# Kernel tuning notes

Hardware: AMD Instinct MI355X
Metric: run time of the kernel (lower is better)

The kernel has to match this reference:

```python
import jax, jax.numpy as jnp
import numpy as np

N_IN, M, CIN, COUT, KVOL = 200000, 600000, 128, 64, 4
BN_EPS = 1e-5


def setup_inputs() -> dict:
    key = jax.random.key(0)
    k1, k2 = jax.random.split(key, 2)
    # Rulebook: transposed conv with kernel=stride=2 means every input voxel i
    # produces KVOL=4 distinct candidate output coords; each output voxel is fed
    # by exactly one (input, kernel-offset) pair. Pick M of the N_IN*KVOL children.
    rng = np.random.RandomState(0)
    perm = rng.permutation(N_IN * KVOL)[:M]
    in_idx = (perm // KVOL).astype(np.int32)   # parent input voxel per output voxel
    kidx = (perm % KVOL).astype(np.int32)      # kernel offset id per output voxel
    feats = jax.random.normal(k1, (N_IN, CIN), jnp.float32)
    weight = jax.random.normal(k2, (KVOL, CIN, COUT), jnp.float32) * (1.0 / np.sqrt(CIN * KVOL))
    gamma = jnp.ones((COUT,), jnp.float32)
    beta = jnp.zeros((COUT,), jnp.float32)
    return dict(feats=feats, weight=weight, gamma=gamma, beta=beta,
                in_idx=jnp.asarray(in_idx), kidx=jnp.asarray(kidx))


def reference(feats, weight, gamma, beta, in_idx, kidx):
    # Sparse transposed conv: gather parent features, apply per-offset GEMM, select.
    gathered = feats[in_idx]                                  # [M, Cin]
    out = jnp.zeros((in_idx.shape[0], weight.shape[2]), feats.dtype)
    for k in range(weight.shape[0]):                          # KVOL=4 structurally distinct weights
        out = out + jnp.where((kidx == k)[:, None], gathered @ weight[k], 0.0)
    # BatchNorm1d (training-mode batch stats over voxel dim) + ReLU
    mean = out.mean(axis=0)
    var = out.var(axis=0)                                     # biased, as torch BN uses
    y = (out - mean) * jax.lax.rsqrt(var + BN_EPS) * gamma + beta
    return jax.nn.relu(y)
```

## Files before the change

### kernel.cpp

```cpp
#include <hip/hip_runtime.h>

#define CIN  128
#define COUT 64
#define KVOL 4
#define TP   128
#define BN_EPS 1e-5f

typedef __bf16 bf16x8 __attribute__((ext_vector_type(8)));
typedef float  f32x4  __attribute__((ext_vector_type(4)));
typedef float  f32x8  __attribute__((ext_vector_type(8)));


__global__ void k_prepw(const float* __restrict__ weight, __bf16* __restrict__ wfrag) {
  int id = blockIdx.x * 256 + threadIdx.x;
  int j  = id & 7;
  int l  = (id >> 3) & 63;
  int ks = (id >> 9) & 3;
  int f  = (id >> 11) & 3;
  int k  = id >> 13;
  int kk = ks * 32 + (l >> 4) * 8 + j;
  int n  = 4 * (l & 15) + f;
  wfrag[id] = (__bf16)weight[(k * CIN + kk) * COUT + n];
}

__global__ void k_fill(int4* __restrict__ p, long n4) {
  long i = (long)blockIdx.x * blockDim.x + threadIdx.x;
  long stride = (long)gridDim.x * blockDim.x;
  int4 v = make_int4(-1, -1, -1, -1);
  for (; i < n4; i += stride) p[i] = v;
}

__global__ void k_tbl(const int* __restrict__ in_idx, const int* __restrict__ kidx,
                      int M, int N_IN, int* __restrict__ tbl_t) {
  for (int m = blockIdx.x * blockDim.x + threadIdx.x; m < M;
       m += gridDim.x * blockDim.x)
    tbl_t[(kidx[m] & 3) * N_IN + in_idx[m]] = m;
}

__device__ inline int4 ld_mk(const int* __restrict__ tbl_t, int k, int N_IN, int pi) {
  int4 mk;
  if (pi + 3 < N_IN) {
    mk = *(const int4*)&tbl_t[k * N_IN + pi];
  } else {
    mk.x = (pi + 0 < N_IN) ? tbl_t[k * N_IN + pi + 0] : -1;
    mk.y = (pi + 1 < N_IN) ? tbl_t[k * N_IN + pi + 1] : -1;
    mk.z = (pi + 2 < N_IN) ? tbl_t[k * N_IN + pi + 2] : -1;
    mk.w = (pi + 3 < N_IN) ? tbl_t[k * N_IN + pi + 3] : -1;
  }
  return mk;
}

__global__ __launch_bounds__(256, 4)
void k_pass1(const float* __restrict__ feats, const int* __restrict__ tbl_t,
             const __bf16* __restrict__ wfrag, float* __restrict__ pbuf, int N_IN) {
  __shared__ float red[512];
  int t  = threadIdx.x;
  int w  = t >> 6, l = t & 63;
  int lr = l & 15, lg = l >> 4;
  int base = blockIdx.x * TP + w * 32;

  bf16x8 a[2][4];
  #pragma unroll
  for (int mf = 0; mf < 2; ++mf) {
    int row = base + mf * 16 + lr;
    bool vr = row < N_IN;
    const float* ap = feats + (long)(vr ? row : 0) * CIN + lg * 8;
    #pragma unroll
    for (int ks = 0; ks < 4; ++ks) {
      f32x8 fv = {0.f,0.f,0.f,0.f,0.f,0.f,0.f,0.f};
      if (vr) fv = *(const f32x8*)(ap + ks * 32);
      a[mf][ks] = __builtin_convertvector(fv, bf16x8);
    }
  }

  float s[4] = {0.f,0.f,0.f,0.f}, q[4] = {0.f,0.f,0.f,0.f};
  int pi0 = base + lg * 4;
  int pi1 = base + 16 + lg * 4;

  #pragma unroll 1
  for (int k = 0; k < KVOL; ++k) {
    int4 mk0 = ld_mk(tbl_t, k, N_IN, pi0);
    int4 mk1 = ld_mk(tbl_t, k, N_IN, pi1);
    const bf16x8* wp = (const bf16x8*)wfrag + k * 1024 + l;
    f32x4 acc[2][4];
    #pragma unroll
    for (int mf = 0; mf < 2; ++mf)
      #pragma unroll
      for (int f = 0; f < 4; ++f) acc[mf][f] = (f32x4){0.f, 0.f, 0.f, 0.f};
    #pragma unroll
    for (int ks = 0; ks < 4; ++ks)
      #pragma unroll
      for (int f = 0; f < 4; ++f) {
        bf16x8 b = wp[(f * 4 + ks) * 64];
        acc[0][f] = __builtin_amdgcn_mfma_f32_16x16x32_bf16(a[0][ks], b, acc[0][f], 0, 0, 0);
        acc[1][f] = __builtin_amdgcn_mfma_f32_16x16x32_bf16(a[1][ks], b, acc[1][f], 0, 0, 0);
      }
    #pragma unroll
    for (int mf = 0; mf < 2; ++mf) {
      int4 mk = mf ? mk1 : mk0;
      #pragma unroll
      for (int reg = 0; reg < 4; ++reg) {
        int m = (reg == 0) ? mk.x : (reg == 1) ? mk.y : (reg == 2) ? mk.z : mk.w;
        if (m >= 0) {
          #pragma unroll
          for (int f = 0; f < 4; ++f) {
            float vv = acc[mf][f][reg];
            s[f] += vv; q[f] += vv * vv;
          }
        }
      }
    }
  }

  #pragma unroll
  for (int f = 0; f < 4; ++f) {
    s[f] += __shfl_xor(s[f], 16); s[f] += __shfl_xor(s[f], 32);
    q[f] += __shfl_xor(q[f], 16); q[f] += __shfl_xor(q[f], 32);
  }
  float* redS = red;
  float* redQ = red + 256;
  if (lg == 0) {
    #pragma unroll
    for (int f = 0; f < 4; ++f) {
      redS[w * 64 + 4 * lr + f] = s[f];
      redQ[w * 64 + 4 * lr + f] = q[f];
    }
  }
  __syncthreads();
  if (t < 128) {
    int col = t & 63;
    const float* src = (t < 64) ? redS : redQ;
    float v = 0.f;
    #pragma unroll
    for (int g = 0; g < 4; ++g) v += src[g * 64 + col];
    pbuf[(long)blockIdx.x * 128 + t] = v;
  }
}

__global__ void k_stats(const float* __restrict__ pbuf, int nb,
                        float* __restrict__ gsum, float* __restrict__ gsq) {
  __shared__ float red[256];
  int j = blockIdx.x;
  float v = 0.f;
  for (int r = threadIdx.x; r < nb; r += blockDim.x)
    v += pbuf[(long)r * 128 + j];
  red[threadIdx.x] = v;
  __syncthreads();
  #pragma unroll
  for (int sft = 128; sft > 0; sft >>= 1) {
    if (threadIdx.x < sft) red[threadIdx.x] += red[threadIdx.x + sft];
    __syncthreads();
  }
  if (threadIdx.x == 0) {
    if (j < 64) gsum[j] = red[0];
    else        gsq[j - 64] = red[0];
  }
}

__global__ __launch_bounds__(256, 4)
void k_pass2(const float* __restrict__ feats, const int* __restrict__ tbl_t,
             const __bf16* __restrict__ wfrag, float* __restrict__ out,
             const float* __restrict__ gsum, const float* __restrict__ gsq,
             const float* __restrict__ gamma, const float* __restrict__ beta,
             int N_IN, int M) {
  int t  = threadIdx.x;
  int w  = t >> 6, l = t & 63;
  int lr = l & 15, lg = l >> 4;
  int base = blockIdx.x * TP + w * 32;

  float inv = 1.0f / (float)M;
  f32x4 sm = *(const f32x4*)&gsum[4 * lr];
  f32x4 sq = *(const f32x4*)&gsq[4 * lr];
  f32x4 ga = *(const f32x4*)&gamma[4 * lr];
  f32x4 be = *(const f32x4*)&beta[4 * lr];
  float sc[4], sh[4];
  #pragma unroll
  for (int f = 0; f < 4; ++f) {
    float mu = sm[f] * inv;
    float r  = rsqrtf(sq[f] * inv - mu * mu + BN_EPS);
    sc[f] = r * ga[f];
    sh[f] = be[f] - mu * sc[f];
  }

  bf16x8 a[2][4];
  #pragma unroll
  for (int mf = 0; mf < 2; ++mf) {
    int row = base + mf * 16 + lr;
    bool vr = row < N_IN;
    const float* ap = feats + (long)(vr ? row : 0) * CIN + lg * 8;
    #pragma unroll
    for (int ks = 0; ks < 4; ++ks) {
      f32x8 fv = {0.f,0.f,0.f,0.f,0.f,0.f,0.f,0.f};
      if (vr) fv = *(const f32x8*)(ap + ks * 32);
      a[mf][ks] = __builtin_convertvector(fv, bf16x8);
    }
  }

  int pi0 = base + lg * 4;
  int pi1 = base + 16 + lg * 4;

  #pragma unroll 1
  for (int k = 0; k < KVOL; ++k) {
    int4 mk0 = ld_mk(tbl_t, k, N_IN, pi0);
    int4 mk1 = ld_mk(tbl_t, k, N_IN, pi1);
    const bf16x8* wp = (const bf16x8*)wfrag + k * 1024 + l;
    f32x4 acc[2][4];
    #pragma unroll
    for (int mf = 0; mf < 2; ++mf)
      #pragma unroll
      for (int f = 0; f < 4; ++f) acc[mf][f] = (f32x4){0.f, 0.f, 0.f, 0.f};
    #pragma unroll
    for (int ks = 0; ks < 4; ++ks)
      #pragma unroll
      for (int f = 0; f < 4; ++f) {
        bf16x8 b = wp[(f * 4 + ks) * 64];
        acc[0][f] = __builtin_amdgcn_mfma_f32_16x16x32_bf16(a[0][ks], b, acc[0][f], 0, 0, 0);
        acc[1][f] = __builtin_amdgcn_mfma_f32_16x16x32_bf16(a[1][ks], b, acc[1][f], 0, 0, 0);
      }
    #pragma unroll
    for (int mf = 0; mf < 2; ++mf) {
      int4 mk = mf ? mk1 : mk0;
      #pragma unroll
      for (int reg = 0; reg < 4; ++reg) {
        int m = (reg == 0) ? mk.x : (reg == 1) ? mk.y : (reg == 2) ? mk.z : mk.w;
        if (m >= 0) {
          f32x4 v4;
          #pragma unroll
          for (int f = 0; f < 4; ++f)
            v4[f] = fmaxf(fmaf(acc[mf][f][reg], sc[f], sh[f]), 0.f);
          __builtin_nontemporal_store(v4, (f32x4*)&out[(long)m * COUT + 4 * lr]);
        }
      }
    }
  }
}

extern "C" void kernel_launch(void* const* d_in, const int* in_sizes, int n_in,
                              void* d_out, int out_size, void* d_ws, size_t ws_size,
                              hipStream_t stream) {
  const float* feats  = (const float*)d_in[0];
  const float* weight = (const float*)d_in[1];
  const float* gamma  = (const float*)d_in[2];
  const float* beta   = (const float*)d_in[3];
  const int*   in_idx = (const int*)d_in[4];
  const int*   kidx   = (const int*)d_in[5];
  int M    = in_sizes[4];
  int N_IN = in_sizes[0] / CIN;
  float* out = (float*)d_out;

  int nb = (N_IN + TP - 1) / TP;

  float*  gsum  = (float*)((char*)d_ws + 128);
  float*  gsq   = (float*)((char*)d_ws + 384);
  __bf16* wfrag = (__bf16*)((char*)d_ws + 1024);
  int*    tbl_t = (int*)((char*)d_ws + 66560);
  size_t  pbuf_off = 66560 + (size_t)N_IN * KVOL * sizeof(int);
  float*  pbuf  = (float*)((char*)d_ws + pbuf_off);

  long n4 = (long)N_IN * KVOL / 4;
  k_fill<<<1024, 256, 0, stream>>>((int4*)tbl_t, n4);
  k_prepw<<<128, 256, 0, stream>>>(weight, wfrag);
  k_tbl<<<1024, 256, 0, stream>>>(in_idx, kidx, M, N_IN, tbl_t);

  k_pass1<<<nb, 256, 0, stream>>>(feats, tbl_t, wfrag, pbuf, N_IN);
  k_stats<<<128, 256, 0, stream>>>(pbuf, nb, gsum, gsq);
  k_pass2<<<nb, 256, 0, stream>>>(feats, tbl_t, wfrag, out, gsum, gsq, gamma, beta,
                                  N_IN, M);
}
```

Before: 111.5 us.

## Restructure BN-apply pass to iterate over output voxels with gathered inputs

```diff
diff --git a/kernel.cpp b/kernel.cpp
--- a/kernel.cpp
+++ b/kernel.cpp
@@ -50,6 +50,8 @@
   return mk;
 }
 
+__device__ inline bf16x8 sel8(bool c, bf16x8 a, bf16x8 z) { return c ? a : z; }
+
 __global__ __launch_bounds__(256, 4)
 void k_pass1(const float* __restrict__ feats, const int* __restrict__ tbl_t,
              const __bf16* __restrict__ wfrag, float* __restrict__ pbuf, int N_IN) {
@@ -158,15 +160,17 @@
 }
 
 __global__ __launch_bounds__(256, 4)
-void k_pass2(const float* __restrict__ feats, const int* __restrict__ tbl_t,
-             const __bf16* __restrict__ wfrag, float* __restrict__ out,
-             const float* __restrict__ gsum, const float* __restrict__ gsq,
-             const float* __restrict__ gamma, const float* __restrict__ beta,
-             int N_IN, int M) {
+void k_pass2m(const float* __restrict__ feats, const int* __restrict__ in_idx,
+              const int* __restrict__ kidx, const __bf16* __restrict__ wfrag,
+              float* __restrict__ out,
+              const float* __restrict__ gsum, const float* __restrict__ gsq,
+              const float* __restrict__ gamma, const float* __restrict__ beta,
+              int M) {
+  __shared__ char Fl[4][32 * 256];
   int t  = threadIdx.x;
   int w  = t >> 6, l = t & 63;
   int lr = l & 15, lg = l >> 4;
-  int base = blockIdx.x * TP + w * 32;
+  int base = blockIdx.x * 128 + w * 32;
 
   float inv = 1.0f / (float)M;
   f32x4 sm = *(const f32x4*)&gsum[4 * lr];
@@ -182,57 +186,77 @@
     sh[f] = be[f] - mu * sc[f];
   }
 
+  {
+    int r = l >> 1, h = l & 1;
+    int m = base + r;
+    bool v = m < M;
+    int g = v ? in_idx[m] : 0;
+    const float* src = feats + (long)g * CIN + h * 64;
+    char* dst = Fl[w] + r * 256;
+    int sw = (r & 7) << 4;
+    #pragma unroll
+    for (int i = 0; i < 8; ++i) {
+      f32x8 fv = {0.f,0.f,0.f,0.f,0.f,0.f,0.f,0.f};
+      if (v) fv = *(const f32x8*)(src + i * 8);
+      *(bf16x8*)(dst + ((h * 128 + i * 16) ^ sw)) = __builtin_convertvector(fv, bf16x8);
+    }
+  }
+  __syncthreads();
+
+  int m0 = base + lr, m1 = base + 16 + lr;
+  int kA0 = (m0 < M) ? (kidx[m0] & 3) : -1;
+  int kA1 = (m1 < M) ? (kidx[m1] & 3) : -1;
+
   bf16x8 a[2][4];
   #pragma unroll
   for (int mf = 0; mf < 2; ++mf) {
-    int row = base + mf * 16 + lr;
-    bool vr = row < N_IN;
-    const float* ap = feats + (long)(vr ? row : 0) * CIN + lg * 8;
-    #pragma unroll
-    for (int ks = 0; ks < 4; ++ks) {
-      f32x8 fv = {0.f,0.f,0.f,0.f,0.f,0.f,0.f,0.f};
-      if (vr) fv = *(const f32x8*)(ap + ks * 32);
-      a[mf][ks] = __builtin_convertvector(fv, bf16x8);
-    }
-  }
-
-  int pi0 = base + lg * 4;
-  int pi1 = base + 16 + lg * 4;
+    int r = mf * 16 + lr;
+    const char* ap = Fl[w] + r * 256;
+    int sw = (r & 7) << 4;
+    #pragma unroll
+    for (int ks = 0; ks < 4; ++ks)
+      a[mf][ks] = *(const bf16x8*)(ap + ((ks * 64 + lg * 16) ^ sw));
+  }
+
+  f32x8 zf = {0.f,0.f,0.f,0.f,0.f,0.f,0.f,0.f};
+  bf16x8 z8 = __builtin_convertvector(zf, bf16x8);
+
+  f32x4 acc[2][4];
+  #pragma unroll
+  for (int mf = 0; mf < 2; ++mf)
+    #pragma unroll
+    for (int f = 0; f < 4; ++f) acc[mf][f] = (f32x4){0.f, 0.f, 0.f, 0.f};
 
   #pragma unroll 1
   for (int k = 0; k < KVOL; ++k) {
-    int4 mk0 = ld_mk(tbl_t, k, N_IN, pi0);
-    int4 mk1 = ld_mk(tbl_t, k, N_IN, pi1);
     const bf16x8* wp = (const bf16x8*)wfrag + k * 1024 + l;
-    f32x4 acc[2][4];
-    #pragma unroll
-    for (int mf = 0; mf < 2; ++mf)
-      #pragma unroll
-      for (int f = 0; f < 4; ++f) acc[mf][f] = (f32x4){0.f, 0.f, 0.f, 0.f};
-    #pragma unroll
-    for (int ks = 0; ks < 4; ++ks)
+    bool s0 = (kA0 == k), s1 = (kA1 == k);
+    #pragma unroll
+    for (int ks = 0; ks < 4; ++ks) {
+      bf16x8 a0 = sel8(s0, a[0][ks], z8);
+      bf16x8 a1 = sel8(s1, a[1][ks], z8);
       #pragma unroll
       for (int f = 0; f < 4; ++f) {
         bf16x8 b = wp[(f * 4 + ks) * 64];
-        acc[0][f] = __builtin_amdgcn_mfma_f32_16x16x32_bf16(a[0][ks], b, acc[0][f], 0, 0, 0);
-        acc[1][f] = __builtin_amdgcn_mfma_f32_16x16x32_bf16(a[1][ks], b, acc[1][f], 0, 0, 0);
-      }
-    #pragma unroll
-    for (int mf = 0; mf < 2; ++mf) {
-      int4 mk = mf ? mk1 : mk0;
-      #pragma unroll
-      for (int reg = 0; reg < 4; ++reg) {
-        int m = (reg == 0) ? mk.x : (reg == 1) ? mk.y : (reg == 2) ? mk.z : mk.w;
-        if (m >= 0) {
-          f32x4 v4;
-          #pragma unroll
-          for (int f = 0; f < 4; ++f)
-            v4[f] = fmaxf(fmaf(acc[mf][f][reg], sc[f], sh[f]), 0.f);
-          __builtin_nontemporal_store(v4, (f32x4*)&out[(long)m * COUT + 4 * lr]);
-        }
-      }
-    }
-  }
+        acc[0][f] = __builtin_amdgcn_mfma_f32_16x16x32_bf16(a0, b, acc[0][f], 0, 0, 0);
+        acc[1][f] = __builtin_amdgcn_mfma_f32_16x16x32_bf16(a1, b, acc[1][f], 0, 0, 0);
+      }
+    }
+  }
+
+  #pragma unroll
+  for (int mf = 0; mf < 2; ++mf)
+    #pragma unroll
+    for (int reg = 0; reg < 4; ++reg) {
+      int m = base + mf * 16 + lg * 4 + reg;
+      if (m < M) {
+        f32x4 v4;
+        #pragma unroll
+        for (int f = 0; f < 4; ++f)
+          v4[f] = fmaxf(fmaf(acc[mf][f][reg], sc[f], sh[f]), 0.f);
+        __builtin_nontemporal_store(v4, (f32x4*)&out[(long)m * COUT + 4 * lr]);
+      }
+    }
 }
 
 extern "C" void kernel_launch(void* const* d_in, const int* in_sizes, int n_in,
@@ -264,6 +288,8 @@
 
   k_pass1<<<nb, 256, 0, stream>>>(feats, tbl_t, wfrag, pbuf, N_IN);
   k_stats<<<128, 256, 0, stream>>>(pbuf, nb, gsum, gsq);
-  k_pass2<<<nb, 256, 0, stream>>>(feats, tbl_t, wfrag, out, gsum, gsq, gamma, beta,
-                                  N_IN, M);
-}
+
+  int nb2 = (M + 127) / 128;
+  k_pass2m<<<nb2, 256, 0, stream>>>(feats, in_idx, kidx, wfrag, out,
+                                    gsum, gsq, gamma, beta, M);
+}
```

After: 202.3 us. 1.82x slower.
